# Kernel tuning notes

Measured on AMD Instinct MI355X. Metric: run time of the kernel, lower is better.

## Reference

```python
import jax, jax.numpy as jnp
import numpy as np
import math


def setup_inputs() -> dict:
    key = jax.random.key(0)
    ks = jax.random.split(key, 10)
    b, n, d, h = 2, 1024, 1024, 16
    hd = d // h
    std = 0.02
    x = jax.random.normal(ks[0], (b, n, d), jnp.float32)
    Wq = jax.random.normal(ks[1], (d, d), jnp.float32) * std
    Wk = jax.random.normal(ks[2], (d, d), jnp.float32) * std
    Wv = jax.random.normal(ks[3], (d, d), jnp.float32) * std
    Wo = jax.random.normal(ks[4], (d, d), jnp.float32) * std
    Ww1 = jax.random.normal(ks[5], (d, hd), jnp.float32) * std
    Ww2 = jax.random.normal(ks[6], (hd, d), jnp.float32) * std
    Wb = jax.random.normal(ks[7], (d, h), jnp.float32) * std
    Wf = jax.random.normal(ks[8], (d, h), jnp.float32) * std
    # delta initialized so sigmoid(delta) = threshold = 0.99
    delta = jnp.full((h,), math.log(0.99 / (1.0 - 0.99)), jnp.float32)
    return dict(x=x, Wq=Wq, Wk=Wk, Wv=Wv, Wo=Wo, Ww1=Ww1, Ww2=Ww2, Wb=Wb, Wf=Wf, delta=delta)


def reference(x, Wq, Wk, Wv, Wo, Ww1, Ww2, Wb, Wf, delta):
    b, n, d = x.shape
    h = delta.shape[0]
    hd = d // h
    scale = hd ** -0.5
    q = (x @ Wq).reshape(b, n, h, hd)
    k = (x @ Wk).reshape(b, n, h, hd)
    v = (x @ Wv).reshape(b, n, h, hd)
    w = ((x @ Ww1) @ Ww2).reshape(b, n, h, hd)
    # l2-normalize write directions per head
    w = w * jax.lax.rsqrt(jnp.sum(w * w, axis=-1, keepdims=True) + 1e-6)
    beta = 2.0 * jax.nn.sigmoid(x @ Wb)                      # (b,n,h)
    log_f = jax.nn.log_sigmoid((x @ Wf + delta).astype(jnp.float32))  # (b,n,h)
    bt = jnp.transpose(beta, (0, 2, 1))                      # (b,h,n)
    # PaTH attention: logit_{t,j} = q_t^T H_t H_{t-1} ... H_{j+1} k_j, H_s = I - beta_s w_s w_s^T.
    # UT transform: c_{s,j} = w_s . k_j^{(s-1)} satisfies (I + L) C = tril(W K^T, -1)
    # with L_{s,r} = beta_r (w_s . w_r) for r < s.
    A = jnp.einsum('bshd,brhd->bhsr', w, w)                  # w_s . w_r
    L = jnp.tril(A, -1) * bt[:, :, None, :]                  # (b,h,n,n), strictly lower
    Mlow = jnp.tril(jnp.einsum('bshd,bjhd->bhsj', w, k), -1)
    C = jax.scipy.linalg.solve_triangular(L, Mlow, lower=True, unit_diagonal=True)
    # transformed score: S_{t,j} = q_t.k_j - sum_{j<s<=t} beta_s (q_t.w_s) c_{s,j}
    G = jnp.tril(jnp.einsum('bthd,bshd->bhts', q, w) * bt[:, :, None, :])
    S = jnp.einsum('bthd,bjhd->bhtj', q, k) - G @ C          # (b,h,n,n)
    # forgetting-gate decay: add F_t - F_j (cumulative log-sigmoid gates)
    Fc = jnp.cumsum(jnp.transpose(log_f, (0, 2, 1)), axis=-1)  # (b,h,n)
    logits = S * scale + Fc[..., :, None] - Fc[..., None, :]
    mask = jnp.tril(jnp.ones((n, n), bool))
    logits = jnp.where(mask, logits, -jnp.inf)
    P = jax.nn.softmax(logits, axis=-1)
    o = jnp.einsum('bhtj,bjhd->bthd', P, v).reshape(b, n, d)
    return o @ Wo
```

## Files before the change

kernel.cpp:

```cpp
#include <hip/hip_runtime.h>
#include <hip/hip_bf16.h>

#define DEV static __device__ __forceinline__

constexpr float SM_SCALE = 0.125f;

typedef __attribute__((ext_vector_type(8))) short s16x8;
typedef __attribute__((ext_vector_type(8))) unsigned short u16x8;
typedef __attribute__((ext_vector_type(4))) unsigned short u16x4;
typedef __attribute__((ext_vector_type(4))) float f32x4;

DEV float bf2f(unsigned short u) {
  union { unsigned int i; float f; } v; v.i = ((unsigned int)u) << 16; return v.f;
}
DEV unsigned short f2bf(float f) {
  union { float f; unsigned int i; } v; v.f = f;
  unsigned int r = v.i + 0x7fffu + ((v.i >> 16) & 1u);
  return (unsigned short)(r >> 16);
}
DEV void tri_unrank(int r, int& k, int& i) {
  k = (int)((sqrtf(8.f * r + 1.f) - 1.f) * 0.5f);
  while (k * (k + 1) / 2 > r) --k;
  while ((k + 1) * (k + 2) / 2 <= r) ++k;
  i = r - k * (k + 1) / 2;
}
DEV void glds16(const void* g, void* l) {
  __builtin_amdgcn_global_load_lds(
      (const __attribute__((address_space(1))) void*)g,
      (__attribute__((address_space(3))) void*)l, 16, 0, 0);
}
DEV void pipe_drain_barrier() {
  asm volatile("s_waitcnt vmcnt(0)" ::: "memory");
  __builtin_amdgcn_s_barrier();
}

constexpr size_t OFF_XB   = 0;
constexpr size_t OFF_WQT  = 4194304;
constexpr size_t OFF_WKT  = 6291456;
constexpr size_t OFF_WVT  = 8388608;
constexpr size_t OFF_WOT  = 10485760;
constexpr size_t OFF_W1C  = 12582912;
constexpr size_t OFF_W2T  = 12713984;
constexpr size_t OFF_BETA = 12582912;
constexpr size_t OFF_Q16  = 12845056;
constexpr size_t OFF_K16  = 17039360;
constexpr size_t OFF_VT   = 21233664;
constexpr size_t OFF_WN16 = 25427968;
constexpr size_t OFF_WB16 = 29622272;
constexpr size_t OFF_WNF  = 33816576;
constexpr size_t OFF_OB   = 33816576;
constexpr size_t OFF_BFT  = 38010880;
constexpr size_t OFF_FC   = 38273024;
constexpr size_t OFF_L    = 38404096;
constexpr size_t OFF_CT   = 105512960;
constexpr size_t OFF_G    = 172621824;
constexpr size_t OFF_BL   = 239730688;
constexpr size_t OFF_U128 = 244187136;
constexpr size_t OFF_B256 = 252575744;

__global__ __launch_bounds__(256) void prep_all(
    const float* __restrict__ W0, const float* __restrict__ W1,
    const float* __restrict__ W2, const float* __restrict__ W3,
    const float* __restrict__ Ww1, const float* __restrict__ Ww2,
    const float* __restrict__ x, const float* __restrict__ Wb,
    const float* __restrict__ Wf,
    unsigned short* __restrict__ D0, unsigned short* __restrict__ D1,
    unsigned short* __restrict__ D2, unsigned short* __restrict__ D3,
    unsigned short* __restrict__ W1c, unsigned short* __restrict__ W2T,
    unsigned short* __restrict__ xb, unsigned short* __restrict__ BFT) {
  int bidx = blockIdx.x;
  int t = threadIdx.x;
  if (bidx >= 2096) {
    int e0 = ((bidx - 2096) * 256 + t) * 8;
    int j = e0 >> 10, i0 = e0 & 1023;
    u16x8 o;
#pragma unroll
    for (int e = 0; e < 8; ++e) {
      int i = i0 + e;
      float v = 0.f;
      if (j < 16) v = Wb[i * 16 + j];
      else if (j < 32) v = Wf[i * 16 + (j - 16)];
      o[e] = f2bf(v);
    }
    *(u16x8*)(BFT + e0) = o;
    return;
  }
  if (bidx >= 2064) {
    int i = ((bidx - 2064) * 256 + t) * 8;
    float4 a = *(const float4*)(Ww1 + i);
    float4 b = *(const float4*)(Ww1 + i + 4);
    u16x8 o;
    o[0] = f2bf(a.x); o[1] = f2bf(a.y); o[2] = f2bf(a.z); o[3] = f2bf(a.w);
    o[4] = f2bf(b.x); o[5] = f2bf(b.y); o[6] = f2bf(b.z); o[7] = f2bf(b.w);
    *(u16x8*)(W1c + i) = o;
    return;
  }
  if (bidx >= 1040) {
    int i = ((bidx - 1040) * 256 + t) * 8;
    float4 a = *(const float4*)(x + i);
    float4 b = *(const float4*)(x + i + 4);
    u16x8 o;
    o[0] = f2bf(a.x); o[1] = f2bf(a.y); o[2] = f2bf(a.z); o[3] = f2bf(a.w);
    o[4] = f2bf(b.x); o[5] = f2bf(b.y); o[6] = f2bf(b.z); o[7] = f2bf(b.w);
    *(u16x8*)(xb + i) = o;
    return;
  }
  const float* src; unsigned short* dst; int R, C, c0, r0;
  if (bidx >= 1024) {
    src = Ww2; dst = W2T; R = 64; C = 1024;
    c0 = (bidx - 1024) * 64; r0 = 0;
  } else {
    int z = bidx >> 8, xy = bidx & 255;
    src = z == 0 ? W0 : z == 1 ? W1 : z == 2 ? W2 : W3;
    dst = z == 0 ? D0 : z == 1 ? D1 : z == 2 ? D2 : D3;
    R = 1024; C = 1024;
    c0 = (xy & 15) * 64; r0 = (xy >> 4) * 64;
  }
  __shared__ float tile[64 * 65];
#pragma unroll
  for (int i = 0; i < 16; ++i) {
    int lin = t + i * 256; int r = lin >> 6, c = lin & 63;
    tile[r * 65 + c] = src[(size_t)(r0 + r) * C + c0 + c];
  }
  __syncthreads();
#pragma unroll
  for (int i = 0; i < 16; ++i) {
    int lin = t + i * 256; int c = lin >> 6, r = lin & 63;
    dst[(size_t)(c0 + c) * R + r0 + r] = f2bf(tile[r * 65 + c]);
  }
}

__global__ __launch_bounds__(256) void bgfc(const float* __restrict__ BL,
    const float* __restrict__ delta, float* __restrict__ Beta, float* __restrict__ Fc) {
  int bh = blockIdx.x;
  int b = bh >> 4, h = bh & 15;
  int t = threadIdx.x;
  __shared__ float buf[1024];
  __shared__ float tsum[256];
  float dh = delta[h];
#pragma unroll
  for (int i = 0; i < 4; ++i) {
    int n = t + i * 256;
    int row = (b << 10) + n;
    float braw = BL[row * 64 + h];
    Beta[row * 16 + h] = 2.f / (1.f + __expf(-braw));
    float lraw = BL[row * 64 + 16 + h] + dh;
    buf[n] = (lraw >= 0.f) ? -log1pf(__expf(-lraw)) : (lraw - log1pf(__expf(lraw)));
  }
  __syncthreads();
  float loc[4]; float run = 0.f;
#pragma unroll
  for (int i = 0; i < 4; ++i) { run += buf[t * 4 + i]; loc[i] = run; }
  tsum[t] = run;
  __syncthreads();
  for (int off = 1; off < 256; off <<= 1) {
    float add = (t >= off) ? tsum[t - off] : 0.f;
    __syncthreads();
    tsum[t] += add;
    __syncthreads();
  }
  float excl = tsum[t] - run;
#pragma unroll
  for (int i = 0; i < 4; ++i) Fc[bh * 1024 + t * 4 + i] = excl + loc[i];
}

__global__ __launch_bounds__(256) void proj_big(const unsigned short* __restrict__ xb,
    const unsigned short* __restrict__ WqT, const unsigned short* __restrict__ WkT,
    const unsigned short* __restrict__ WvT, const unsigned short* __restrict__ WfT,
    const unsigned short* __restrict__ BFT,
    unsigned short* __restrict__ Q16, unsigned short* __restrict__ K16,
    unsigned short* __restrict__ VT, unsigned short* __restrict__ WNF,
    float* __restrict__ BL) {
  int idx = blockIdx.x;
  const unsigned short *A, *BT; unsigned short* out = nullptr; int m0, n0;
  int mode = 0;
  if (idx < 256) {
    int my = idx >> 4, nx = idx & 15;
    m0 = my * 128; A = xb;
    if (nx < 8) { BT = WqT; out = Q16; n0 = nx * 128; }
    else { BT = WkT; out = K16; n0 = (nx - 8) * 128; }
  } else if (idx < 384) {
    int r = idx - 256; int bz = r >> 6; int rem = r & 63;
    m0 = (rem >> 3) * 128; n0 = (rem & 7) * 128;
    A = WvT; BT = xb + ((size_t)bz << 20); out = VT + ((size_t)bz << 20);
  } else if (idx < 512) {
    int r2 = idx - 384;
    m0 = (r2 >> 3) * 128; n0 = (r2 & 7) * 128;
    A = xb; BT = WfT; out = WNF;
  } else {
    m0 = (idx - 512) * 128; n0 = 0;
    A = xb; BT = BFT; mode = 1;
  }
  int t = threadIdx.x;
  int w = t >> 6, l = t & 63;
  int wr = w >> 1, wc = w & 1;
  int fr = l & 15, fq = l >> 4;
  __shared__ unsigned short As[2 * 8192];
  __shared__ unsigned short Bs[2 * 8192];
  f32x4 acc[4][4];
#pragma unroll
  for (int m = 0; m < 4; ++m)
#pragma unroll
    for (int c = 0; c < 4; ++c) acc[m][c] = (f32x4){0.f, 0.f, 0.f, 0.f};

#define STAGE_PB(buf, k0) {                                             \
  _Pragma("unroll")                                                     \
  for (int i = 0; i < 4; ++i) {                                         \
    int cid = t + i * 256;                                              \
    int row = cid >> 3, ch = cid & 7;                                   \
    int chs = ch ^ (row & 7);                                           \
    glds16(A + (size_t)(m0 + row) * 1024 + (k0) + chs * 8, (char*)(As + (buf) * 8192) + cid * 16); \
    glds16(BT + (size_t)(n0 + row) * 1024 + (k0) + chs * 8, (char*)(Bs + (buf) * 8192) + cid * 16); \
  } }

  STAGE_PB(0, 0);
  pipe_drain_barrier();
  int cur = 0;
  for (int kt = 0; kt < 16; ++kt) {
    if (kt < 15) STAGE_PB(cur ^ 1, (kt + 1) * 64);
    const char* Ab = (const char*)(As + cur * 8192);
    const char* Bb = (const char*)(Bs + cur * 8192);
    __builtin_amdgcn_s_setprio(1);
#pragma unroll
    for (int kh = 0; kh < 2; ++kh) {
      s16x8 af[4], bfv[4];
#pragma unroll
      for (int m = 0; m < 4; ++m) {
        int ra = wr * 64 + 16 * m + fr;
        af[m] = *(const s16x8*)(Ab + (((ra << 7) + (kh << 6) + (fq << 4)) ^ ((ra & 7) << 4)));
      }
#pragma unroll
      for (int c = 0; c < 4; ++c) {
        int rb = wc * 64 + 16 * c + fr;
        bfv[c] = *(const s16x8*)(Bb + (((rb << 7) + (kh << 6) + (fq << 4)) ^ ((rb & 7) << 4)));
      }
#pragma unroll
      for (int m = 0; m < 4; ++m)
#pragma unroll
        for (int c = 0; c < 4; ++c)
          acc[m][c] = __builtin_amdgcn_mfma_f32_16x16x32_bf16(af[m], bfv[c], acc[m][c], 0, 0, 0);
    }
    __builtin_amdgcn_s_setprio(0);
    pipe_drain_barrier();
    cur ^= 1;
  }
#undef STAGE_PB
#pragma unroll
  for (int m = 0; m < 4; ++m) {
#pragma unroll
    for (int c = 0; c < 4; ++c) {
      int col = n0 + wc * 64 + 16 * c + fr;
#pragma unroll
      for (int r = 0; r < 4; ++r) {
        int grow = m0 + wr * 64 + 16 * m + fq * 4 + r;
        if (mode == 0) out[(size_t)grow * 1024 + col] = f2bf(acc[m][c][r]);
        else if (col < 64) BL[(size_t)grow * 64 + col] = acc[m][c][r];
      }
    }
  }
}

template<int F32OUT>
__global__ __launch_bounds__(256) void gemm_nt(const unsigned short* __restrict__ A,
    const unsigned short* __restrict__ BT, void* __restrict__ out,
    int M, int N, int K) {
  __shared__ unsigned short As[2 * 4096];
  __shared__ unsigned short Bs[2 * 4096];
  int m0 = blockIdx.y * 64, n0 = blockIdx.x * 64;
  int t = threadIdx.x;
  int w = t >> 6, l = t & 63, fr = l & 15;
  int koB = (l >> 4) * 16;
  f32x4 acc[4];
#pragma unroll
  for (int c = 0; c < 4; ++c) acc[c] = (f32x4){0.f, 0.f, 0.f, 0.f};

#define STAGE_G(buf, k0) {                                              \
  _Pragma("unroll")                                                     \
  for (int i = 0; i < 2; ++i) {                                         \
    int cid = t + i * 256;                                              \
    int row = cid >> 3, ch = cid & 7;                                   \
    int chs = ch ^ (row & 7);                                           \
    glds16(A + (size_t)(m0 + row) * K + (k0) + chs * 8, (char*)(As + (buf) * 4096) + cid * 16); \
    glds16(BT + (size_t)(n0 + row) * K + (k0) + chs * 8, (char*)(Bs + (buf) * 4096) + cid * 16); \
  } }

  int nt = K >> 6;
  STAGE_G(0, 0);
  pipe_drain_barrier();
  int cur = 0;
  for (int kt = 0; kt < nt; ++kt) {
    if (kt + 1 < nt) STAGE_G(cur ^ 1, (kt + 1) * 64);
    const char* Ab = (const char*)(As + cur * 4096);
    const char* Bb = (const char*)(Bs + cur * 4096);
    __builtin_amdgcn_s_setprio(1);
#pragma unroll
    for (int kh = 0; kh < 2; ++kh) {
      int ra = 16 * w + fr;
      s16x8 a = *(const s16x8*)(Ab + (((ra << 7) + (kh << 6) + koB) ^ ((ra & 7) << 4)));
#pragma unroll
      for (int c = 0; c < 4; ++c) {
        int rb = 16 * c + fr;
        s16x8 bb = *(const s16x8*)(Bb + (((rb << 7) + (kh << 6) + koB) ^ ((rb & 7) << 4)));
        acc[c] = __builtin_amdgcn_mfma_f32_16x16x32_bf16(a, bb, acc[c], 0, 0, 0);
      }
    }
    __builtin_amdgcn_s_setprio(0);
    pipe_drain_barrier();
    cur ^= 1;
  }
#undef STAGE_G
  int rbase = m0 + 16 * w + ((l >> 4) << 2);
#pragma unroll
  for (int c = 0; c < 4; ++c) {
    int col = n0 + 16 * c + fr;
#pragma unroll
    for (int r = 0; r < 4; ++r) {
      if (F32OUT) ((float*)out)[(size_t)(rbase + r) * N + col] = acc[c][r];
      else ((unsigned short*)out)[(size_t)(rbase + r) * N + col] = f2bf(acc[c][r]);
    }
  }
}

__global__ __launch_bounds__(256) void wnorm2(const unsigned short* __restrict__ WNF,
    const float* __restrict__ Beta, unsigned short* __restrict__ WN,
    unsigned short* __restrict__ WB) {
  int row = blockIdx.x;
  int wave = threadIdx.x >> 6, lane = threadIdx.x & 63;
#pragma unroll
  for (int i = 0; i < 4; ++i) {
    int hh = wave * 4 + i;
    size_t idx = ((size_t)row << 10) + hh * 64 + lane;
    float v = bf2f(WNF[idx]);
    float ss = v * v;
#pragma unroll
    for (int off = 1; off < 64; off <<= 1) ss += __shfl_xor(ss, off);
    float wn = v * rsqrtf(ss + 1e-6f);
    WN[idx] = f2bf(wn);
    WB[idx] = f2bf(wn * Beta[row * 16 + hh]);
  }
}

__global__ __launch_bounds__(256) void pairLG(const unsigned short* __restrict__ WN,
    const unsigned short* __restrict__ Q, const unsigned short* __restrict__ WB,
    unsigned short* __restrict__ Lg, unsigned short* __restrict__ Gg) {
  int idx = blockIdx.x;
  int bh = idx & 31, r0r = idx >> 5;
  int tb2, jb2; tri_unrank(r0r, tb2, jb2);
  int b = bh >> 4, h = bh & 15;
  int m0 = tb2 * 128, n0 = jb2 * 128;
  int t = threadIdx.x;
  int w = t >> 6, l = t & 63;
  int wr = w >> 1, wc = w & 1;
  int fr = l & 15, fq = l >> 4;
  __shared__ unsigned short As[128 * 64];
  __shared__ unsigned short Bs[128 * 64];
  const unsigned short* WNb = WN + ((size_t)b << 20) + h * 64;
  const unsigned short* Qb  = Q + ((size_t)b << 20) + h * 64;
  const unsigned short* WBb = WB + ((size_t)b << 20) + h * 64;
  size_t base = (size_t)bh << 20;
#pragma unroll
  for (int i = 0; i < 4; ++i) {
    int cid = t + i * 256;
    int row = cid >> 3, ch = cid & 7;
    int chs = ch ^ (row & 7);
    glds16(WNb + ((size_t)(m0 + row) << 10) + chs * 8, (char*)As + cid * 16);
    glds16(WBb + ((size_t)(n0 + row) << 10) + chs * 8, (char*)Bs + cid * 16);
  }
  __syncthreads();
  for (int pass = 0; pass < 2; ++pass) {
    f32x4 acc[4][4];
#pragma unroll
    for (int m = 0; m < 4; ++m)
#pragma unroll
      for (int c = 0; c < 4; ++c) acc[m][c] = (f32x4){0.f, 0.f, 0.f, 0.f};
#pragma unroll
    for (int kh = 0; kh < 2; ++kh) {
      s16x8 af[4], bfv[4];
#pragma unroll
      for (int m = 0; m < 4; ++m) {
        int ra = wr * 64 + 16 * m + fr;
        af[m] = *(const s16x8*)((char*)As + (((ra << 7) + (kh << 6) + (fq << 4)) ^ ((ra & 7) << 4)));
      }
#pragma unroll
      for (int c = 0; c < 4; ++c) {
        int rb = wc * 64 + 16 * c + fr;
        bfv[c] = *(const s16x8*)((char*)Bs + (((rb << 7) + (kh << 6) + (fq << 4)) ^ ((rb & 7) << 4)));
      }
#pragma unroll
      for (int m = 0; m < 4; ++m)
#pragma unroll
        for (int c = 0; c < 4; ++c)
          acc[m][c] = __builtin_amdgcn_mfma_f32_16x16x32_bf16(af[m], bfv[c], acc[m][c], 0, 0, 0);
    }
    unsigned short* dst = pass ? Gg : Lg;
#pragma unroll
    for (int m = 0; m < 4; ++m) {
#pragma unroll
      for (int c = 0; c < 4; ++c) {
        int gj = n0 + wc * 64 + 16 * c + fr;
#pragma unroll
        for (int r = 0; r < 4; ++r) {
          int gi = m0 + wr * 64 + 16 * m + fq * 4 + r;
          bool keep = pass ? (gj <= gi) : (gj < gi);
          dst[base + ((size_t)gi << 10) + gj] = f2bf(keep ? -acc[m][c][r] : 0.f);
        }
      }
    }
    if (pass == 0) {
      __syncthreads();
#pragma unroll
      for (int i = 0; i < 4; ++i) {
        int cid = t + i * 256;
        int row = cid >> 3, ch = cid & 7;
        int chs = ch ^ (row & 7);
        glds16(Qb + ((size_t)(m0 + row) << 10) + chs * 8, (char*)As + cid * 16);
      }
      __syncthreads();
    }
  }
}

__global__ __launch_bounds__(256) void score128s(const unsigned short* __restrict__ Q,
    const unsigned short* __restrict__ Kk, const unsigned short* __restrict__ G,
    const unsigned short* __restrict__ CT, unsigned short* __restrict__ Sg) {
  int idx = blockIdx.x;
  int bh = idx & 31, r0r = idx >> 5;
  int k, i; tri_unrank(r0r, k, i);
  int tb2 = (7 - k) + i, jb2 = i;
  int b = bh >> 4, h = bh & 15;
  int m0 = tb2 * 128, n0 = jb2 * 128;
  int t = threadIdx.x;
  int w = t >> 6, l = t & 63;
  int wr = w >> 1, wc = w & 1;
  int fr = l & 15, fq = l >> 4;
  __shared__ unsigned short As[2 * 8192];
  __shared__ unsigned short Bs[2 * 8192];
  size_t base = (size_t)bh << 20;
  const unsigned short* Qb_ = Q + ((size_t)b << 20) + h * 64;
  const unsigned short* Kb_ = Kk + ((size_t)b << 20) + h * 64;
  const unsigned short* Gb_ = G + base;
  const unsigned short* Cb_ = CT + base;
  int kbase = jb2 * 128;
  int nsteps = 1 + (tb2 - jb2 + 1) * 2;
  f32x4 acc[4][4];
#pragma unroll
  for (int m = 0; m < 4; ++m)
#pragma unroll
    for (int c = 0; c < 4; ++c) acc[m][c] = (f32x4){0.f, 0.f, 0.f, 0.f};

#define STAGE_SC(buf, stp) {                                            \
  const unsigned short* pa; const unsigned short* pb; int koff;         \
  if ((stp) == 0) { pa = Qb_; pb = Kb_; koff = 0; }                     \
  else { pa = Gb_; pb = Cb_; koff = kbase + ((stp) - 1) * 64; }         \
  _Pragma("unroll")                                                     \
  for (int i2 = 0; i2 < 4; ++i2) {                                      \
    int cid = t + i2 * 256;                                             \
    int row = cid >> 3, ch = cid & 7;                                   \
    int chs = ch ^ (row & 7);                                           \
    glds16(pa + ((size_t)(m0 + row) << 10) + koff + chs * 8, (char*)(As + (buf) * 8192) + cid * 16); \
    glds16(pb + ((size_t)(n0 + row) << 10) + koff + chs * 8, (char*)(Bs + (buf) * 8192) + cid * 16); \
  } }

  STAGE_SC(0, 0);
  pipe_drain_barrier();
  int cur = 0;
  for (int step = 0; step < nsteps; ++step) {
    if (step + 1 < nsteps) STAGE_SC(cur ^ 1, step + 1);
    const char* Ab = (const char*)(As + cur * 8192);
    const char* Bb = (const char*)(Bs + cur * 8192);
    __builtin_amdgcn_s_setprio(1);
#pragma unroll
    for (int kh = 0; kh < 2; ++kh) {
      s16x8 af[4], bfv[4];
#pragma unroll
      for (int m = 0; m < 4; ++m) {
        int ra = wr * 64 + 16 * m + fr;
        af[m] = *(const s16x8*)(Ab + (((ra << 7) + (kh << 6) + (fq << 4)) ^ ((ra & 7) << 4)));
      }
#pragma unroll
      for (int c = 0; c < 4; ++c) {
        int rb = wc * 64 + 16 * c + fr;
        bfv[c] = *(const s16x8*)(Bb + (((rb << 7) + (kh << 6) + (fq << 4)) ^ ((rb & 7) << 4)));
      }
#pragma unroll
      for (int m = 0; m < 4; ++m)
#pragma unroll
        for (int c = 0; c < 4; ++c)
          acc[m][c] = __builtin_amdgcn_mfma_f32_16x16x32_bf16(af[m], bfv[c], acc[m][c], 0, 0, 0);
    }
    __builtin_amdgcn_s_setprio(0);
    pipe_drain_barrier();
    cur ^= 1;
  }
#undef STAGE_SC
#pragma unroll
  for (int m = 0; m < 4; ++m) {
#pragma unroll
    for (int c = 0; c < 4; ++c) {
      int gj = n0 + wc * 64 + 16 * c + fr;
#pragma unroll
      for (int r = 0; r < 4; ++r) {
        int gi = m0 + wr * 64 + 16 * m + fq * 4 + r;
        Sg[base + ((size_t)gi << 10) + gj] = f2bf(acc[m][c][r]);
      }
    }
  }
}

__global__ __launch_bounds__(256) void invbuild(const unsigned short* __restrict__ Lb,
    unsigned short* __restrict__ U128) {
  int ib = blockIdx.x, bh = blockIdx.y;
  int t = threadIdx.x, w = t >> 6, l = t & 63, fr = l & 15, fq = l >> 4;
  int s0 = ib * 128;
  size_t base = (size_t)bh << 20;
  unsigned short* Uo = U128 + (((size_t)(bh * 8 + ib)) << 14);
  __shared__ float LD[2][64 * 65];
  __shared__ unsigned short UaR[64 * 72];
  __shared__ unsigned short UcR[64 * 72];
  __shared__ unsigned short UaT[64 * 64];
  __shared__ unsigned short T1T[64 * 64];
#pragma unroll
  for (int i = 0; i < 32; ++i) {
    int lin = t + i * 256;
    int blk = lin >> 12, s = (lin >> 6) & 63, r = lin & 63;
    LD[blk][s * 65 + r] = -bf2f(Lb[base + ((size_t)(s0 + blk * 64 + s) << 10) + s0 + blk * 64 + r]);
  }
  __syncthreads();
  if (t < 128) {
    int blk = t >> 6, j = t & 63;
    const float* ld = LD[blk];
    float cc[64];
#pragma unroll
    for (int s = 0; s < 64; ++s) cc[s] = (s == j) ? 1.f : 0.f;
#pragma unroll
    for (int r = 0; r < 63; ++r) {
      float val = cc[r];
#pragma unroll
      for (int s = r + 1; s < 64; ++s) cc[s] -= ld[s * 65 + r] * val;
    }
    if (blk == 0) {
#pragma unroll
      for (int s = 0; s < 64; ++s) {
        unsigned short v = f2bf(cc[s]);
        UaR[s * 72 + j] = v;
        *(unsigned short*)((char*)UaT + (((j << 7) + (s << 1)) ^ ((j & 7) << 4))) = v;
      }
    } else {
#pragma unroll
      for (int s = 0; s < 64; ++s) UcR[s * 72 + j] = f2bf(cc[s]);
    }
  }
  __syncthreads();
#pragma unroll
  for (int i = 0; i < 8; ++i) {
    int cid = t + i * 256;
    int row = cid >> 4, ch = cid & 15;
    u16x8 v = {0, 0, 0, 0, 0, 0, 0, 0};
    if (row < 64) {
      if (ch < 8) {
#pragma unroll
        for (int e = 0; e < 8; ++e) v[e] = UaR[row * 72 + ch * 8 + e];
      }
      *(u16x8*)(Uo + row * 128 + ch * 8) = v;
    } else if (ch >= 8) {
#pragma unroll
      for (int e = 0; e < 8; ++e) v[e] = UcR[(row - 64) * 72 + (ch - 8) * 8 + e];
      *(u16x8*)(Uo + row * 128 + ch * 8) = v;
    }
  }
  f32x4 a1[4];
#pragma unroll
  for (int c = 0; c < 4; ++c) a1[c] = (f32x4){0.f, 0.f, 0.f, 0.f};
#pragma unroll
  for (int kc = 0; kc < 2; ++kc) {
    s16x8 af = *(const s16x8*)(Lb + base + ((size_t)(s0 + 64 + 16 * w + fr) << 10) + s0 + kc * 32 + fq * 8);
#pragma unroll
    for (int c = 0; c < 4; ++c) {
      int j = 16 * c + fr;
      s16x8 bb = *(const s16x8*)((char*)UaT + (((j << 7) + (kc << 6) + (fq << 4)) ^ ((j & 7) << 4)));
      a1[c] = __builtin_amdgcn_mfma_f32_16x16x32_bf16(af, bb, a1[c], 0, 0, 0);
    }
  }
#pragma unroll
  for (int c = 0; c < 4; ++c) {
    int gj = 16 * c + fr;
    int sb = 16 * w + fq * 4;
    u16x4 pk;
#pragma unroll
    for (int r = 0; r < 4; ++r) pk[r] = f2bf(a1[c][r]);
    *(u16x4*)((char*)T1T + (((gj << 7) + (sb << 1)) ^ ((gj & 7) << 4))) = pk;
  }
  __syncthreads();
  f32x4 a2[4];
#pragma unroll
  for (int c = 0; c < 4; ++c) a2[c] = (f32x4){0.f, 0.f, 0.f, 0.f};
#pragma unroll
  for (int kc = 0; kc < 2; ++kc) {
    s16x8 af = *(const s16x8*)(UcR + (16 * w + fr) * 72 + kc * 32 + fq * 8);
#pragma unroll
    for (int c = 0; c < 4; ++c) {
      int j = 16 * c + fr;
      s16x8 bb = *(const s16x8*)((char*)T1T + (((j << 7) + (kc << 6) + (fq << 4)) ^ ((j & 7) << 4)));
      a2[c] = __builtin_amdgcn_mfma_f32_16x16x32_bf16(af, bb, a2[c], 0, 0, 0);
    }
  }
#pragma unroll
  for (int c = 0; c < 4; ++c) {
    int gj = 16 * c + fr;
#pragma unroll
    for (int r = 0; r < 4; ++r)
      Uo[(64 + 16 * w + fq * 4 + r) * 128 + gj] = f2bf(a2[c][r]);
  }
}

__global__ __launch_bounds__(256) void u256build(const unsigned short* __restrict__ Lb,
    const unsigned short* __restrict__ U128, unsigned short* __restrict__ B256) {
  int qb = blockIdx.x, bh = blockIdx.y;
  int t = threadIdx.x, w = t >> 6, l = t & 63, fr = l & 15, fq = l >> 4;
  int s0 = qb * 256;
  size_t base = (size_t)bh << 20;
  const unsigned short* Ua = U128 + (((size_t)(bh * 8 + 2 * qb)) << 14);
  const unsigned short* Uc = U128 + (((size_t)(bh * 8 + 2 * qb + 1)) << 14);
  unsigned short* out = B256 + (((size_t)(bh * 4 + qb)) << 14);
  __shared__ unsigned short UaT[16384];
  __shared__ unsigned short T1T[16384];
#pragma unroll
  for (int i = 0; i < 8; ++i) {
    int cid = t + i * 256;
    int s = cid >> 4, ch = cid & 15;
    u16x8 v = *(const u16x8*)(Ua + s * 128 + ch * 8);
#pragma unroll
    for (int e = 0; e < 8; ++e) {
      int j = ch * 8 + e;
      int byt = ((j << 8) + (s << 1)) ^ ((j & 15) << 4);
      *(unsigned short*)((char*)UaT + byt) = v[e];
    }
  }
  __syncthreads();
  f32x4 a1[2][8];
#pragma unroll
  for (int m = 0; m < 2; ++m)
#pragma unroll
    for (int c = 0; c < 8; ++c) a1[m][c] = (f32x4){0.f, 0.f, 0.f, 0.f};
#pragma unroll
  for (int kc = 0; kc < 4; ++kc) {
    s16x8 af[2];
#pragma unroll
    for (int m = 0; m < 2; ++m)
      af[m] = *(const s16x8*)(Lb + base + ((size_t)(s0 + 128 + 32 * w + 16 * m + fr) << 10) + s0 + kc * 32 + fq * 8);
#pragma unroll
    for (int c = 0; c < 8; ++c) {
      int j = 16 * c + fr;
      s16x8 bb = *(const s16x8*)((char*)UaT + (((j << 8) + (kc << 6) + (fq << 4)) ^ ((j & 15) << 4)));
#pragma unroll
      for (int m = 0; m < 2; ++m)
        a1[m][c] = __builtin_amdgcn_mfma_f32_16x16x32_bf16(af[m], bb, a1[m][c], 0, 0, 0);
    }
  }
#pragma unroll
  for (int m = 0; m < 2; ++m) {
#pragma unroll
    for (int c = 0; c < 8; ++c) {
      int col = 16 * c + fr;
      int row0 = 32 * w + 16 * m + fq * 4;
      u16x4 pk;
#pragma unroll
      for (int r = 0; r < 4; ++r) pk[r] = f2bf(a1[m][c][r]);
      int byt = ((col << 8) + (row0 << 1)) ^ ((col & 15) << 4);
      *(u16x4*)((char*)T1T + byt) = pk;
    }
  }
  __syncthreads();
  f32x4 a2[2][8];
#pragma unroll
  for (int m = 0; m < 2; ++m)
#pragma unroll
    for (int c = 0; c < 8; ++c) a2[m][c] = (f32x4){0.f, 0.f, 0.f, 0.f};
#pragma unroll
  for (int kc = 0; kc < 4; ++kc) {
    s16x8 af[2];
#pragma unroll
    for (int m = 0; m < 2; ++m)
      af[m] = *(const s16x8*)(Uc + (32 * w + 16 * m + fr) * 128 + kc * 32 + fq * 8);
#pragma unroll
    for (int c = 0; c < 8; ++c) {
      int j = 16 * c + fr;
      s16x8 bb = *(const s16x8*)((char*)T1T + (((j << 8) + (kc << 6) + (fq << 4)) ^ ((j & 15) << 4)));
#pragma unroll
      for (int m = 0; m < 2; ++m)
        a2[m][c] = __builtin_amdgcn_mfma_f32_16x16x32_bf16(af[m], bb, a2[m][c], 0, 0, 0);
    }
  }
#pragma unroll
  for (int m = 0; m < 2; ++m) {
#pragma unroll
    for (int c = 0; c < 8; ++c) {
      int col = 16 * c + fr;
#pragma unroll
      for (int r = 0; r < 4; ++r)
        out[(32 * w + 16 * m + fq * 4 + r) * 128 + col] = f2bf(a2[m][c][r]);
    }
  }
}

__global__ __launch_bounds__(256) void solve256(const unsigned short* __restrict__ WN,
    const unsigned short* __restrict__ Kk, const unsigned short* __restrict__ Lb,
    const unsigned short* __restrict__ U128, const unsigned short* __restrict__ B256,
    unsigned short* __restrict__ CT, int ib) {
  int jb = blockIdx.x, bh = blockIdx.y;
  int b = bh >> 4, h = bh & 15;
  int t = threadIdx.x, w = t >> 6, l = t & 63, fr = l & 15, fq = l >> 4;
  int s0 = ib * 256, j0 = jb * 128;
  size_t base = (size_t)bh << 20;
  __shared__ unsigned short sh[49152];
  unsigned short* rT = sh;
  const unsigned short* Wb_ = WN + ((size_t)b << 20) + h * 64;
  const unsigned short* Kb_ = Kk + ((size_t)b << 20) + h * 64;

  f32x4 acc[4][8];
#pragma unroll
  for (int m = 0; m < 4; ++m)
#pragma unroll
    for (int c = 0; c < 8; ++c) acc[m][c] = (f32x4){0.f, 0.f, 0.f, 0.f};
  int nst = 1 + 4 * ib - 2 * jb; if (nst < 1) nst = 1;

#define STAGE_SV(buf, stp) {                                            \
  int rb = 2 * jb + (stp) - 1;                                          \
  _Pragma("unroll")                                                     \
  for (int i = 0; i < 8; ++i) {                                         \
    int cid = t + i * 256;                                              \
    int row = cid >> 3, ch = cid & 7;                                   \
    int chs = ch ^ (row & 7);                                           \
    const unsigned short* ga = ((stp) == 0)                             \
      ? Wb_ + ((size_t)(s0 + row) << 10) + chs * 8                      \
      : Lb + base + ((size_t)(s0 + row) << 10) + rb * 64 + chs * 8;     \
    glds16(ga, (char*)(sh + (buf) * 16384) + cid * 16);                 \
  }                                                                     \
  _Pragma("unroll")                                                     \
  for (int i = 0; i < 4; ++i) {                                         \
    int cid = t + i * 256;                                              \
    int row = cid >> 3, ch = cid & 7;                                   \
    int chs = ch ^ (row & 7);                                           \
    const unsigned short* gb = ((stp) == 0)                             \
      ? Kb_ + ((size_t)(j0 + row) << 10) + chs * 8                      \
      : CT + base + ((size_t)(j0 + row) << 10) + rb * 64 + chs * 8;     \
    glds16(gb, (char*)(sh + 32768 + (buf) * 8192) + cid * 16);          \
  } }

  STAGE_SV(0, 0);
  pipe_drain_barrier();
  int cur = 0;
  for (int st = 0; st < nst; ++st) {
    if (st + 1 < nst) STAGE_SV(cur ^ 1, st + 1);
    const char* Ab = (const char*)(sh + cur * 16384);
    const char* Bb = (const char*)(sh + 32768 + cur * 8192);
    __builtin_amdgcn_s_setprio(1);
#pragma unroll
    for (int kh = 0; kh < 2; ++kh) {
      s16x8 af[4], bfv[8];
#pragma unroll
      for (int m = 0; m < 4; ++m) {
        int ra = 64 * w + 16 * m + fr;
        af[m] = *(const s16x8*)(Ab + (((ra << 7) + (kh << 6) + (fq << 4)) ^ ((ra & 7) << 4)));
      }
#pragma unroll
      for (int c = 0; c < 8; ++c) {
        int rb2 = 16 * c + fr;
        bfv[c] = *(const s16x8*)(Bb + (((rb2 << 7) + (kh << 6) + (fq << 4)) ^ ((rb2 & 7) << 4)));
      }
#pragma unroll
      for (int m = 0; m < 4; ++m)
#pragma unroll
        for (int c = 0; c < 8; ++c)
          acc[m][c] = __builtin_amdgcn_mfma_f32_16x16x32_bf16(af[m], bfv[c], acc[m][c], 0, 0, 0);
    }
    __builtin_amdgcn_s_setprio(0);
    pipe_drain_barrier();
    cur ^= 1;
  }
#undef STAGE_SV
#pragma unroll
  for (int m = 0; m < 4; ++m) {
#pragma unroll
    for (int c = 0; c < 8; ++c) {
      int sl0 = 64 * w + 16 * m + fq * 4;
      int jl = 16 * c + fr;
      u16x4 pk;
#pragma unroll
      for (int r = 0; r < 4; ++r) {
        float v = acc[m][c][r];
        if (j0 + jl >= s0 + sl0 + r) v = 0.f;
        pk[r] = f2bf(v);
      }
      int byt = ((jl << 9) + (sl0 << 1)) ^ ((jl & 15) << 4);
      *(u16x4*)((char*)rT + byt) = pk;
    }
  }
  __syncthreads();
  const unsigned short* Ua = U128 + (((size_t)(bh * 8 + 2 * ib)) << 14);
  const unsigned short* Uc = U128 + (((size_t)(bh * 8 + 2 * ib + 1)) << 14);
  const unsigned short* Bm = B256 + (((size_t)(bh * 4 + ib)) << 14);
#pragma unroll
  for (int m = 0; m < 4; ++m)
#pragma unroll
    for (int c = 0; c < 8; ++c) acc[m][c] = (f32x4){0.f, 0.f, 0.f, 0.f};
  int nkc = (w < 2) ? 4 : 8;
  for (int kc = 0; kc < nkc; ++kc) {
    const unsigned short* src; int arow;
    if (w < 2) { src = Ua; arow = 64 * w; }
    else { src = (kc < 4) ? Bm : Uc; arow = 64 * (w - 2); }
    s16x8 uf[4];
#pragma unroll
    for (int m = 0; m < 4; ++m)
      uf[m] = *(const s16x8*)(src + (arow + 16 * m + fr) * 128 + (kc & 3) * 32 + fq * 8);
#pragma unroll
    for (int c = 0; c < 8; ++c) {
      int jl = 16 * c + fr;
      s16x8 bb = *(const s16x8*)((char*)rT + (((jl << 9) + (kc << 6) + (fq << 4)) ^ ((jl & 15) << 4)));
#pragma unroll
      for (int m = 0; m < 4; ++m)
        acc[m][c] = __builtin_amdgcn_mfma_f32_16x16x32_bf16(uf[m], bb, acc[m][c], 0, 0, 0);
    }
  }
#pragma unroll
  for (int m = 0; m < 4; ++m) {
#pragma unroll
    for (int c = 0; c < 8; ++c) {
      int jl = 16 * c + fr;
      int sb = 64 * w + 16 * m + fq * 4;
      u16x4 pk;
#pragma unroll
      for (int r = 0; r < 4; ++r) pk[r] = f2bf(acc[m][c][r]);
      *(u16x4*)(CT + base + ((size_t)(j0 + jl) << 10) + s0 + sb) = pk;
    }
  }
}

__global__ __launch_bounds__(256) void pv_kernel(const unsigned short* __restrict__ S,
    const unsigned short* __restrict__ VT, const float* __restrict__ Fc,
    unsigned short* __restrict__ Ob) {
  int idx = blockIdx.x;
  int bh = idx & 31, rank = idx >> 5;
  int tb = 15 - rank;
  int b = bh >> 4, h = bh & 15;
  int t0 = tb * 64;
  int t = threadIdx.x, w = t >> 6, l = t & 63, fr = l & 15, fq = l >> 4;
  __shared__ unsigned short Pl[64 * 64];
  __shared__ float mrow[64], lrow[64], crow[64];
  if (t < 64) { mrow[t] = -1e30f; lrow[t] = 0.f; }
  size_t base = (size_t)bh << 20;
  f32x4 acc[4];
#pragma unroll
  for (int c = 0; c < 4; ++c) acc[c] = (f32x4){0.f,0.f,0.f,0.f};
  for (int jb = 0; jb <= tb; ++jb) {
    int j0 = jb * 64;
    __syncthreads();
    float vals[2][8], tmax[2];
#pragma unroll
    for (int i = 0; i < 2; ++i) {
      int cid = t + i * 256;
      int row = cid >> 3, ch = cid & 7;
      int grow = t0 + row;
      u16x8 sv = *(const u16x8*)(S + base + ((size_t)grow << 10) + j0 + ch * 8);
      float4 f0 = *(const float4*)(Fc + bh * 1024 + j0 + ch * 8);
      float4 f1 = *(const float4*)(Fc + bh * 1024 + j0 + ch * 8 + 4);
      float tm = -1e30f;
#pragma unroll
      for (int e = 0; e < 8; ++e) {
        float fc = e < 4 ? ((const float*)&f0)[e] : ((const float*)&f1)[e - 4];
        float v = bf2f(sv[e]) * SM_SCALE - fc;
        if (jb == tb && ch * 8 + e > row) v = -1e30f;
        vals[i][e] = v; tm = fmaxf(tm, v);
      }
      tm = fmaxf(tm, __shfl_xor(tm, 1));
      tm = fmaxf(tm, __shfl_xor(tm, 2));
      tm = fmaxf(tm, __shfl_xor(tm, 4));
      tmax[i] = tm;
    }
    if ((t & 7) == 0) {
#pragma unroll
      for (int i = 0; i < 2; ++i) {
        int row = (t >> 3) + i * 32;
        float mo = mrow[row];
        float mn = fmaxf(mo, tmax[i]);
        float sc = __expf(mo - mn);
        crow[row] = sc; mrow[row] = mn;
        lrow[row] *= sc;
      }
    }
    __syncthreads();
    float ps[2];
#pragma unroll
    for (int i = 0; i < 2; ++i) {
      int cid = t + i * 256;
      int row = cid >> 3, ch = cid & 7;
      float mn = mrow[row];
      u16x8 pv;
      float psum = 0.f;
#pragma unroll
      for (int e = 0; e < 8; ++e) {
        float p = __expf(vals[i][e] - mn);
        psum += p; pv[e] = f2bf(p);
      }
      int byt = ((row << 7) + (ch << 4)) ^ ((row & 7) << 4);
      *(u16x8*)((char*)Pl + byt) = pv;
      psum += __shfl_xor(psum, 1);
      psum += __shfl_xor(psum, 2);
      psum += __shfl_xor(psum, 4);
      ps[i] = psum;
    }
    if ((t & 7) == 0) {
      lrow[t >> 3] += ps[0];
      lrow[(t >> 3) + 32] += ps[1];
    }
    __syncthreads();
    float cr[4];
#pragma unroll
    for (int r = 0; r < 4; ++r) cr[r] = crow[16 * w + fq * 4 + r];
#pragma unroll
    for (int c = 0; c < 4; ++c)
#pragma unroll
      for (int r = 0; r < 4; ++r) acc[c][r] *= cr[r];
#pragma unroll
    for (int kh = 0; kh < 2; ++kh) {
      int ra = 16 * w + fr;
      s16x8 a = *(const s16x8*)((char*)Pl + (((ra << 7) + (kh << 6) + (fq << 4)) ^ ((ra & 7) << 4)));
#pragma unroll
      for (int c = 0; c < 4; ++c) {
        s16x8 bb = *(const s16x8*)(VT + ((size_t)bh * 64 + 16 * c + fr) * 1024 + j0 + kh * 32 + fq * 8);
        acc[c] = __builtin_amdgcn_mfma_f32_16x16x32_bf16(a, bb, acc[c], 0, 0, 0);
      }
    }
  }
  __syncthreads();
  float inv[4];
#pragma unroll
  for (int r = 0; r < 4; ++r) inv[r] = 1.f / lrow[16 * w + fq * 4 + r];
#pragma unroll
  for (int c = 0; c < 4; ++c) {
#pragma unroll
    for (int r = 0; r < 4; ++r) {
      int grow = t0 + 16 * w + fq * 4 + r;
      Ob[((size_t)(b * 1024) + grow) * 1024 + h * 64 + 16 * c + fr] = f2bf(acc[c][r] * inv[r]);
    }
  }
}

extern "C" void kernel_launch(void* const* d_in, const int* in_sizes, int n_in,
                              void* d_out, int out_size, void* d_ws, size_t ws_size,
                              hipStream_t stream) {
  const float* x    = (const float*)d_in[0];
  const float* Wq   = (const float*)d_in[1];
  const float* Wk   = (const float*)d_in[2];
  const float* Wv   = (const float*)d_in[3];
  const float* Wo   = (const float*)d_in[4];
  const float* Ww1  = (const float*)d_in[5];
  const float* Ww2  = (const float*)d_in[6];
  const float* Wb   = (const float*)d_in[7];
  const float* Wf   = (const float*)d_in[8];
  const float* delta= (const float*)d_in[9];

  char* ws = (char*)d_ws;
  unsigned short* xb   = (unsigned short*)(ws + OFF_XB);
  unsigned short* WqT  = (unsigned short*)(ws + OFF_WQT);
  unsigned short* WkT  = (unsigned short*)(ws + OFF_WKT);
  unsigned short* WvT  = (unsigned short*)(ws + OFF_WVT);
  unsigned short* WoT  = (unsigned short*)(ws + OFF_WOT);
  unsigned short* W1c  = (unsigned short*)(ws + OFF_W1C);
  unsigned short* W2T  = (unsigned short*)(ws + OFF_W2T);
  float*          Beta = (float*)(ws + OFF_BETA);
  unsigned short* Q16  = (unsigned short*)(ws + OFF_Q16);
  unsigned short* K16  = (unsigned short*)(ws + OFF_K16);
  unsigned short* VT   = (unsigned short*)(ws + OFF_VT);
  unsigned short* WN16 = (unsigned short*)(ws + OFF_WN16);
  unsigned short* WB16 = (unsigned short*)(ws + OFF_WB16);
  unsigned short* WNF16= (unsigned short*)(ws + OFF_WNF);
  unsigned short* ObB  = (unsigned short*)(ws + OFF_OB);
  unsigned short* BFT  = (unsigned short*)(ws + OFF_BFT);
  float*          Fc   = (float*)(ws + OFF_FC);
  unsigned short* Lbuf = (unsigned short*)(ws + OFF_L);
  unsigned short* Sbuf = (unsigned short*)(ws + OFF_L);
  unsigned short* CT   = (unsigned short*)(ws + OFF_CT);
  unsigned short* Gbuf = (unsigned short*)(ws + OFF_G);
  float*          BL   = (float*)(ws + OFF_BL);
  unsigned short* U128 = (unsigned short*)(ws + OFF_U128);
  unsigned short* B256 = (unsigned short*)(ws + OFF_B256);

  dim3 blk(256);
  prep_all<<<2160, blk, 0, stream>>>(Wq, Wk, Wv, Wo, Ww1, Ww2, x, Wb, Wf,
                                     WqT, WkT, WvT, WoT, W1c, W2T, xb, BFT);
  gemm_nt<0><<<dim3(16,16), blk, 0, stream>>>(W2T, W1c, WN16, 1024, 1024, 64);
  proj_big<<<528, blk, 0, stream>>>(xb, WqT, WkT, WvT, WN16, BFT,
                                    Q16, K16, VT, WNF16, BL);
  bgfc<<<32, blk, 0, stream>>>(BL, delta, Beta, Fc);
  wnorm2<<<2048, blk, 0, stream>>>(WNF16, Beta, WN16, WB16);
  pairLG<<<dim3(36 * 32), blk, 0, stream>>>(WN16, Q16, WB16, Lbuf, Gbuf);
  invbuild<<<dim3(8,32), blk, 0, stream>>>(Lbuf, U128);
  u256build<<<dim3(4,32), blk, 0, stream>>>(Lbuf, U128, B256);
  for (int ib = 0; ib < 4; ++ib)
    solve256<<<dim3(2 * ib + 2, 32), blk, 0, stream>>>(WN16, K16, Lbuf, U128, B256, CT, ib);
  score128s<<<dim3(36 * 32), blk, 0, stream>>>(Q16, K16, Gbuf, CT, Sbuf);
  pv_kernel<<<dim3(512), blk, 0, stream>>>(Sbuf, VT, Fc, ObB);
  gemm_nt<1><<<dim3(16,32), blk, 0, stream>>>(ObB, WoT, d_out, 2048, 1024, 1024);
}
```

Baseline: 297.4 us.

## Make PV softmax wave-local, replacing block barriers with register state and shuffles

Each wave now owns its 16 output rows in the PV kernel. The running max and sum live in registers, and the rescale factors are passed by lane shuffles instead of shared-memory arrays. The three __syncthreads per key block are replaced by wave barriers, and the P tile is split into per-wave shared buffers. This removes block-wide synchronisation stalls, at the cost of extra shuffles and a new row-to-thread mapping in the softmax stage that must stay correct.

```diff
diff --git a/kernel.cpp b/kernel.cpp
--- a/kernel.cpp
+++ b/kernel.cpp
@@ -845,97 +845,88 @@
   int b = bh >> 4, h = bh & 15;
   int t0 = tb * 64;
   int t = threadIdx.x, w = t >> 6, l = t & 63, fr = l & 15, fq = l >> 4;
-  __shared__ unsigned short Pl[64 * 64];
-  __shared__ float mrow[64], lrow[64], crow[64];
-  if (t < 64) { mrow[t] = -1e30f; lrow[t] = 0.f; }
+  int g = l >> 3, ch = l & 7;
+  __shared__ unsigned short Pl[4][16 * 64];
   size_t base = (size_t)bh << 20;
+  float m0 = -1e30f, m1 = -1e30f, l0 = 0.f, l1 = 0.f;
   f32x4 acc[4];
 #pragma unroll
   for (int c = 0; c < 4; ++c) acc[c] = (f32x4){0.f,0.f,0.f,0.f};
   for (int jb = 0; jb <= tb; ++jb) {
     int j0 = jb * 64;
-    __syncthreads();
-    float vals[2][8], tmax[2];
+    float sc[2];
 #pragma unroll
     for (int i = 0; i < 2; ++i) {
-      int cid = t + i * 256;
-      int row = cid >> 3, ch = cid & 7;
-      int grow = t0 + row;
+      int row16 = g + i * 8;
+      int row64 = 16 * w + row16;
+      int grow = t0 + row64;
       u16x8 sv = *(const u16x8*)(S + base + ((size_t)grow << 10) + j0 + ch * 8);
       float4 f0 = *(const float4*)(Fc + bh * 1024 + j0 + ch * 8);
       float4 f1 = *(const float4*)(Fc + bh * 1024 + j0 + ch * 8 + 4);
+      float vals[8];
       float tm = -1e30f;
 #pragma unroll
       for (int e = 0; e < 8; ++e) {
         float fc = e < 4 ? ((const float*)&f0)[e] : ((const float*)&f1)[e - 4];
         float v = bf2f(sv[e]) * SM_SCALE - fc;
-        if (jb == tb && ch * 8 + e > row) v = -1e30f;
-        vals[i][e] = v; tm = fmaxf(tm, v);
+        if (jb == tb && ch * 8 + e > row64) v = -1e30f;
+        vals[e] = v; tm = fmaxf(tm, v);
       }
       tm = fmaxf(tm, __shfl_xor(tm, 1));
       tm = fmaxf(tm, __shfl_xor(tm, 2));
       tm = fmaxf(tm, __shfl_xor(tm, 4));
-      tmax[i] = tm;
-    }
-    if ((t & 7) == 0) {
-#pragma unroll
-      for (int i = 0; i < 2; ++i) {
-        int row = (t >> 3) + i * 32;
-        float mo = mrow[row];
-        float mn = fmaxf(mo, tmax[i]);
-        float sc = __expf(mo - mn);
-        crow[row] = sc; mrow[row] = mn;
-        lrow[row] *= sc;
-      }
-    }
-    __syncthreads();
-    float ps[2];
-#pragma unroll
-    for (int i = 0; i < 2; ++i) {
-      int cid = t + i * 256;
-      int row = cid >> 3, ch = cid & 7;
-      float mn = mrow[row];
+      float mo = i ? m1 : m0;
+      float mn = fmaxf(mo, tm);
+      float s = __expf(mo - mn);
       u16x8 pv;
       float psum = 0.f;
 #pragma unroll
       for (int e = 0; e < 8; ++e) {
-        float p = __expf(vals[i][e] - mn);
+        float p = __expf(vals[e] - mn);
         psum += p; pv[e] = f2bf(p);
       }
-      int byt = ((row << 7) + (ch << 4)) ^ ((row & 7) << 4);
-      *(u16x8*)((char*)Pl + byt) = pv;
+      int byt = ((row16 << 7) + (ch << 4)) ^ ((row16 & 7) << 4);
+      *(u16x8*)((char*)Pl[w] + byt) = pv;
       psum += __shfl_xor(psum, 1);
       psum += __shfl_xor(psum, 2);
       psum += __shfl_xor(psum, 4);
-      ps[i] = psum;
-    }
-    if ((t & 7) == 0) {
-      lrow[t >> 3] += ps[0];
-      lrow[(t >> 3) + 32] += ps[1];
-    }
-    __syncthreads();
+      if (i) { m1 = mn; l1 = l1 * s + psum; } else { m0 = mn; l0 = l0 * s + psum; }
+      sc[i] = s;
+    }
+    __builtin_amdgcn_wave_barrier();
     float cr[4];
 #pragma unroll
-    for (int r = 0; r < 4; ++r) cr[r] = crow[16 * w + fq * 4 + r];
+    for (int r = 0; r < 4; ++r) {
+      int rho = fq * 4 + r;
+      int src = (rho & 7) * 8;
+      float v0 = __shfl(sc[0], src);
+      float v1 = __shfl(sc[1], src);
+      cr[r] = (rho < 8) ? v0 : v1;
+    }
 #pragma unroll
     for (int c = 0; c < 4; ++c)
 #pragma unroll
       for (int r = 0; r < 4; ++r) acc[c][r] *= cr[r];
 #pragma unroll
     for (int kh = 0; kh < 2; ++kh) {
-      int ra = 16 * w + fr;
-      s16x8 a = *(const s16x8*)((char*)Pl + (((ra << 7) + (kh << 6) + (fq << 4)) ^ ((ra & 7) << 4)));
+      s16x8 a = *(const s16x8*)((char*)Pl[w] + (((fr << 7) + (kh << 6) + (fq << 4)) ^ ((fr & 7) << 4)));
 #pragma unroll
       for (int c = 0; c < 4; ++c) {
         s16x8 bb = *(const s16x8*)(VT + ((size_t)bh * 64 + 16 * c + fr) * 1024 + j0 + kh * 32 + fq * 8);
         acc[c] = __builtin_amdgcn_mfma_f32_16x16x32_bf16(a, bb, acc[c], 0, 0, 0);
       }
     }
-  }
-  __syncthreads();
+    __builtin_amdgcn_wave_barrier();
+  }
   float inv[4];
 #pragma unroll
-  for (int r = 0; r < 4; ++r) inv[r] = 1.f / lrow[16 * w + fq * 4 + r];
+  for (int r = 0; r < 4; ++r) {
+    int rho = fq * 4 + r;
+    int src = (rho & 7) * 8;
+    float v0 = __shfl(l0, src);
+    float v1 = __shfl(l1, src);
+    inv[r] = 1.f / ((rho < 8) ? v0 : v1);
+  }
 #pragma unroll
   for (int c = 0; c < 4; ++c) {
 #pragma unroll
```

Result: faster. 290.5 us (-2.3%).
